# Kernel tuning notes

Measured on AMD Instinct MI355X. Metric: run time of the kernel, lower is better.

## Reference

```python
import jax, jax.numpy as jnp
import numpy as np

N = 50000      # nodes
E = 800000     # edges (avg degree 16)
IN_DIM = 256
OUT_DIM = 64
HEADS = 4
P_L = 0.1      # freq='low' slope


def setup_inputs() -> dict:
    key = jax.random.key(0)
    ks = jax.random.split(key, 12)
    h = jax.random.normal(ks[0], (N, IN_DIM), dtype=jnp.float32)
    src = jax.random.randint(ks[1], (E,), 0, N, dtype=jnp.int32)
    dst = jax.random.randint(ks[2], (E,), 0, N, dtype=jnp.int32)
    d = jax.random.uniform(ks[3], (N,), dtype=jnp.float32)  # degree norm per node
    s_in = 1.0 / np.sqrt(IN_DIM)
    s_d = 1.0 / np.sqrt(OUT_DIM)
    W_in = jax.random.normal(ks[4], (IN_DIM, HEADS * OUT_DIM), dtype=jnp.float32) * s_in
    b_in = jnp.zeros((HEADS * OUT_DIM,), dtype=jnp.float32)
    W_att = jax.random.normal(ks[5], (HEADS, OUT_DIM, OUT_DIM), dtype=jnp.float32) * s_d
    b_att = jnp.zeros((HEADS, OUT_DIM), dtype=jnp.float32)
    W_g = jax.random.normal(ks[6], (HEADS, 2 * OUT_DIM), dtype=jnp.float32) * s_d
    b_g = jnp.zeros((HEADS,), dtype=jnp.float32)
    W_out = jax.random.normal(ks[7], (HEADS * OUT_DIM, OUT_DIM), dtype=jnp.float32) * s_d
    b_out = jnp.zeros((OUT_DIM,), dtype=jnp.float32)
    return {"h": h, "src": src, "dst": dst, "d": d,
            "W_in": W_in, "b_in": b_in, "W_att": W_att, "b_att": b_att,
            "W_g": W_g, "b_g": b_g, "W_out": W_out, "b_out": b_out}


def reference(h, src, dst, d, W_in, b_in, W_att, b_att, W_g, b_g, W_out, b_out):
    # node transform: [N, H, D]  (dropout is identity in eval mode)
    hh = jax.nn.relu(h @ W_in + b_in).reshape(-1, HEADS, OUT_DIM)
    # per-head att_gate applied at node level (same math as per-edge, cheaper)
    a = jnp.einsum('nhd,hde->nhe', hh, W_att) + b_att           # [N, H, D]
    # gate linear on concat([dst_a, src_a]) split into the two halves of W_g
    g_dst = jnp.einsum('nhd,hd->nh', a, W_g[:, :OUT_DIM])        # [N, H]
    g_src = jnp.einsum('nhd,hd->nh', a, W_g[:, OUT_DIM:])        # [N, H]
    _h = g_dst[dst] + g_src[src] + b_g                           # [E, H]
    # freq='low': relu(where(_h>0, _h, -p_l*_h)) == where(_h>0, _h, -p_l*_h)
    g = jnp.where(_h > 0, _h, -P_L * _h)
    alpha = g * (d[dst] * d[src])[:, None]                       # [E, H]
    msg = hh[src] * alpha[..., None]                             # [E, H, D]
    z = jax.ops.segment_sum(msg, dst, num_segments=N)            # [N, H, D]
    return z.reshape(-1, HEADS * OUT_DIM) @ W_out + b_out        # [N, D]
```

## Files before the change

### kernel.cpp

```cpp
#include <hip/hip_runtime.h>
#include <hip/hip_bf16.h>

#define N_NODES 50000
#define N_EDGES 800000
#define IN_DIM 256
#define OUT_DIM 64
#define HEADS 4
#define HD 256
#define P_L 0.1f
#define TILE_N 64
#define CAP 64
#define OVCAP 4096

typedef __attribute__((ext_vector_type(8))) short bf16x8;
typedef __attribute__((ext_vector_type(4))) float f32x4;

static __device__ __forceinline__ short f2bf(float f) {
    __hip_bfloat16 b = __float2bfloat16(f);
    return *(short*)&b;
}

__global__ __launch_bounds__(256) void precompute_kernel(
    const float* __restrict__ W_att, const float* __restrict__ b_att,
    const float* __restrict__ W_g,
    float* __restrict__ v_dst, float* __restrict__ v_src,
    float* __restrict__ c_dst, float* __restrict__ c_src) {
    int t = threadIdx.x;
    int h = t >> 6, dd = t & 63;
    float sd = 0.f, ss = 0.f;
    for (int e = 0; e < 64; ++e) {
        float w = W_att[h * 4096 + dd * 64 + e];
        sd += w * W_g[h * 128 + e];
        ss += w * W_g[h * 128 + 64 + e];
    }
    v_dst[t] = sd;
    v_src[t] = ss;
    if (dd == 0) {
        float cd = 0.f, cs = 0.f;
        for (int e = 0; e < 64; ++e) {
            float b = b_att[h * 64 + e];
            cd += b * W_g[h * 128 + e];
            cs += b * W_g[h * 128 + 64 + e];
        }
        c_dst[h] = cd;
        c_src[h] = cs;
    }
}

__global__ __launch_bounds__(256) void wconv_kernel(
    const float* __restrict__ W_in, const float* __restrict__ W_out,
    short* __restrict__ W_bt, short* __restrict__ W_obt2) {
    int b = blockIdx.x, t = threadIdx.x;
    if (b < 256) {
        W_bt[t * 256 + b] = f2bf(W_in[b * 256 + t]);
    } else {
        int flat = (b - 256) * 256 + t;
        int k = flat & 63, oc = (flat >> 6) & 63, h = flat >> 12;
        W_obt2[flat] = f2bf(W_out[(h * 64 + k) * 64 + oc]);
    }
}

__global__ __launch_bounds__(256, 2) void node_mfma_kernel(
    const float* __restrict__ hin, const short* __restrict__ W_bt,
    const short* __restrict__ W_obt2, const float* __restrict__ b_in,
    const float* __restrict__ v_dst, const float* __restrict__ v_src,
    const float* __restrict__ c_dst, const float* __restrict__ c_src,
    __hip_bfloat16* __restrict__ y, float* __restrict__ gd,
    float* __restrict__ gs) {
    __shared__ short A_lds[TILE_N * 256];
    int t = threadIdx.x;
    int n0 = blockIdx.x * TILE_N;
    bool full = (n0 + TILE_N) <= N_NODES;

    #pragma unroll
    for (int rr = 0; rr < 4; ++rr) {
        int r = rr * 16 + (t >> 4), c0 = (t & 15) * 16;
        int row = n0 + r;
        if (row > N_NODES - 1) row = N_NODES - 1;
        const float* hp = hin + (size_t)row * IN_DIM + c0;
        float fv[16];
        *(float4*)&fv[0]  = *(const float4*)(hp + 0);
        *(float4*)&fv[4]  = *(const float4*)(hp + 4);
        *(float4*)&fv[8]  = *(const float4*)(hp + 8);
        *(float4*)&fv[12] = *(const float4*)(hp + 12);
        short sv[16];
        #pragma unroll
        for (int j = 0; j < 16; ++j) sv[j] = f2bf(fv[j]);
        int swz = (r & 7) << 3;
        int base = r * 256 + c0;
        *(bf16x8*)&A_lds[(base + 0) ^ swz] = *(bf16x8*)&sv[0];
        *(bf16x8*)&A_lds[(base + 8) ^ swz] = *(bf16x8*)&sv[8];
    }
    __syncthreads();

    int l = t & 63, w = t >> 6;
    int lr = l & 15, lg = l >> 4;
    int aswz = (lr & 7) << 3;

    f32x4 acc[4][4];
    #pragma unroll
    for (int rt = 0; rt < 4; ++rt)
        #pragma unroll
        for (int ct = 0; ct < 4; ++ct) acc[rt][ct] = (f32x4){0.f, 0.f, 0.f, 0.f};

    #pragma unroll
    for (int ks = 0; ks < 8; ++ks) {
        bf16x8 bfrag[4], afrag[4];
        #pragma unroll
        for (int ct = 0; ct < 4; ++ct)
            bfrag[ct] = *(const bf16x8*)(W_bt + (size_t)(w * 64 + ct * 16 + lr) * 256 + ks * 32 + lg * 8);
        #pragma unroll
        for (int rt = 0; rt < 4; ++rt)
            afrag[rt] = *(bf16x8*)&A_lds[((rt * 16 + lr) * 256 + ks * 32 + lg * 8) ^ aswz];
        #pragma unroll
        for (int rt = 0; rt < 4; ++rt)
            #pragma unroll
            for (int ct = 0; ct < 4; ++ct)
                acc[rt][ct] = __builtin_amdgcn_mfma_f32_16x16x32_bf16(afrag[rt], bfrag[ct], acc[rt][ct], 0, 0, 0);
    }

    int col[4];
    float vd[4], vs[4], bi[4];
    #pragma unroll
    for (int ct = 0; ct < 4; ++ct) {
        col[ct] = w * 64 + ct * 16 + lr;
        bi[ct] = b_in[col[ct]];
        vd[ct] = v_dst[col[ct]];
        vs[ct] = v_src[col[ct]];
    }
    float pd[4][4], ps[4][4];
    #pragma unroll
    for (int rt = 0; rt < 4; ++rt)
        #pragma unroll
        for (int r = 0; r < 4; ++r) { pd[rt][r] = 0.f; ps[rt][r] = 0.f; }
    #pragma unroll
    for (int rt = 0; rt < 4; ++rt)
        #pragma unroll
        for (int ct = 0; ct < 4; ++ct)
            #pragma unroll
            for (int r = 0; r < 4; ++r) {
                float v = fmaxf(acc[rt][ct][r] + bi[ct], 0.f);
                acc[rt][ct][r] = v;
                pd[rt][r] += v * vd[ct];
                ps[rt][r] += v * vs[ct];
            }
    #pragma unroll
    for (int rt = 0; rt < 4; ++rt)
        #pragma unroll
        for (int r = 0; r < 4; ++r) {
            #pragma unroll
            for (int off = 1; off < 16; off <<= 1) {
                pd[rt][r] += __shfl_xor(pd[rt][r], off, 64);
                ps[rt][r] += __shfl_xor(ps[rt][r], off, 64);
            }
        }
    if (lr == 0) {
        float cd = c_dst[w], cs = c_src[w];
        #pragma unroll
        for (int rt = 0; rt < 4; ++rt)
            #pragma unroll
            for (int r = 0; r < 4; ++r) {
                int m = rt * 16 + lg * 4 + r;
                if (full || (n0 + m) < N_NODES) {
                    gd[(n0 + m) * HEADS + w] = pd[rt][r] + cd;
                    gs[(n0 + m) * HEADS + w] = ps[rt][r] + cs;
                }
            }
    }

    __syncthreads();
    #pragma unroll
    for (int rt = 0; rt < 4; ++rt)
        #pragma unroll
        for (int ct = 0; ct < 4; ++ct)
            #pragma unroll
            for (int r = 0; r < 4; ++r) {
                int m = rt * 16 + lg * 4 + r;
                int idx = m * 256 + col[ct];
                A_lds[idx ^ (((lg * 4 + r) & 7) << 3)] = f2bf(acc[rt][ct][r]);
            }
    __syncthreads();

    f32x4 acc2[4][4];
    #pragma unroll
    for (int rt = 0; rt < 4; ++rt)
        #pragma unroll
        for (int ct = 0; ct < 4; ++ct) acc2[rt][ct] = (f32x4){0.f, 0.f, 0.f, 0.f};
    #pragma unroll
    for (int ks = 0; ks < 2; ++ks) {
        bf16x8 bfrag[4], afrag[4];
        #pragma unroll
        for (int ct = 0; ct < 4; ++ct)
            bfrag[ct] = *(const bf16x8*)(W_obt2 + (size_t)(w * 64 + ct * 16 + lr) * 64 + ks * 32 + lg * 8);
        #pragma unroll
        for (int rt = 0; rt < 4; ++rt)
            afrag[rt] = *(bf16x8*)&A_lds[((rt * 16 + lr) * 256 + w * 64 + ks * 32 + lg * 8) ^ aswz];
        #pragma unroll
        for (int rt = 0; rt < 4; ++rt)
            #pragma unroll
            for (int ct = 0; ct < 4; ++ct)
                acc2[rt][ct] = __builtin_amdgcn_mfma_f32_16x16x32_bf16(afrag[rt], bfrag[ct], acc2[rt][ct], 0, 0, 0);
    }
    #pragma unroll
    for (int rt = 0; rt < 4; ++rt)
        #pragma unroll
        for (int ct = 0; ct < 4; ++ct)
            #pragma unroll
            for (int r = 0; r < 4; ++r) {
                int m = rt * 16 + lg * 4 + r;
                if (full || (n0 + m) < N_NODES)
                    y[(size_t)(n0 + m) * HD + w * 64 + ct * 16 + lr] =
                        __float2bfloat16(acc2[rt][ct][r]);
            }
}

__global__ __launch_bounds__(256) void fill_kernel(
    const int* __restrict__ src, const int* __restrict__ dst,
    int* __restrict__ cursor, int* __restrict__ bucket_src,
    int* __restrict__ ov_list, int* __restrict__ ov_count) {
    int e = blockIdx.x * 256 + threadIdx.x;
    if (e >= N_EDGES) return;
    int n = dst[e];
    int pos = atomicAdd(&cursor[n], 1);
    if (pos < CAP) {
        bucket_src[(size_t)n * CAP + pos] = src[e];
    } else {
        int oi = atomicAdd(ov_count, 1);
        if (oi < OVCAP) ov_list[oi] = e;
    }
}

__global__ __launch_bounds__(256) void agg_kernel(
    const int* __restrict__ bucket_src, const int* __restrict__ cursor,
    const int* __restrict__ src, const int* __restrict__ dst,
    const int* __restrict__ ov_list, const int* __restrict__ ov_count,
    const float* __restrict__ dnorm, const float* __restrict__ b_g,
    const __hip_bfloat16* __restrict__ y, const float* __restrict__ gd,
    const float* __restrict__ gs, const float* __restrict__ b_out,
    float* __restrict__ out) {
    __shared__ float alpha_lds[4][CAP][HEADS];
    __shared__ int s_lds[4][CAP];
    int t = threadIdx.x;
    int wv = t >> 6, lane = t & 63;
    int n = blockIdx.x * 4 + wv;
    int deg = cursor[n];
    if (deg > CAP) deg = CAP;
    float dn = dnorm[n];

    int hd = lane & 3;
    float gdh = gd[n * HEADS + hd] + b_g[hd];
    #pragma unroll
    for (int it = 0; it < 4; ++it) {
        int ei = it * 16 + (lane >> 2);
        if (ei < deg) {
            int s = bucket_src[(size_t)n * CAP + ei];
            if (hd == 0) s_lds[wv][ei] = s;
            float _h = gdh + gs[s * HEADS + hd];
            float g = _h > 0.f ? _h : -P_L * _h;
            alpha_lds[wv][ei][hd] = g * dn * dnorm[s];
        }
    }
    __syncthreads();

    int h_l = lane >> 4;
    const unsigned int* yw = (const unsigned int*)y + lane * 2;
    float a0 = 0.f, a1 = 0.f, a2 = 0.f, a3 = 0.f;
    int i = 0;
    for (; i + 16 <= deg; i += 16) {
        uint2 v[16];
        float al[16];
        #pragma unroll
        for (int j = 0; j < 16; ++j) {
            int s = s_lds[wv][i + j];
            al[j] = alpha_lds[wv][i + j][h_l];
            v[j] = *(const uint2*)(yw + (size_t)s * 128);
        }
        #pragma unroll
        for (int j = 0; j < 16; ++j) {
            a0 += __uint_as_float(v[j].x << 16) * al[j];
            a1 += __uint_as_float(v[j].x & 0xffff0000u) * al[j];
            a2 += __uint_as_float(v[j].y << 16) * al[j];
            a3 += __uint_as_float(v[j].y & 0xffff0000u) * al[j];
        }
    }
    for (; i + 8 <= deg; i += 8) {
        uint2 v[8];
        float al[8];
        #pragma unroll
        for (int j = 0; j < 8; ++j) {
            int s = s_lds[wv][i + j];
            al[j] = alpha_lds[wv][i + j][h_l];
            v[j] = *(const uint2*)(yw + (size_t)s * 128);
        }
        #pragma unroll
        for (int j = 0; j < 8; ++j) {
            a0 += __uint_as_float(v[j].x << 16) * al[j];
            a1 += __uint_as_float(v[j].x & 0xffff0000u) * al[j];
            a2 += __uint_as_float(v[j].y << 16) * al[j];
            a3 += __uint_as_float(v[j].y & 0xffff0000u) * al[j];
        }
    }
    for (; i < deg; ++i) {
        int s = s_lds[wv][i];
        float al = alpha_lds[wv][i][h_l];
        uint2 vv = *(const uint2*)(yw + (size_t)s * 128);
        a0 += __uint_as_float(vv.x << 16) * al;
        a1 += __uint_as_float(vv.x & 0xffff0000u) * al;
        a2 += __uint_as_float(vv.y << 16) * al;
        a3 += __uint_as_float(vv.y & 0xffff0000u) * al;
    }

    int cnt = *ov_count;
    if (cnt > 0) {
        if (cnt > OVCAP) cnt = OVCAP;
        float gdh2 = gd[n * HEADS + h_l] + b_g[h_l];
        for (int j = 0; j < cnt; ++j) {
            int e = ov_list[j];
            if (dst[e] == n) {
                int s = src[e];
                float _h = gdh2 + gs[s * HEADS + h_l];
                float g = _h > 0.f ? _h : -P_L * _h;
                float al = g * dn * dnorm[s];
                uint2 vv = *(const uint2*)(yw + (size_t)s * 128);
                a0 += __uint_as_float(vv.x << 16) * al;
                a1 += __uint_as_float(vv.x & 0xffff0000u) * al;
                a2 += __uint_as_float(vv.y << 16) * al;
                a3 += __uint_as_float(vv.y & 0xffff0000u) * al;
            }
        }
    }

    a0 += __shfl_xor(a0, 16, 64); a0 += __shfl_xor(a0, 32, 64);
    a1 += __shfl_xor(a1, 16, 64); a1 += __shfl_xor(a1, 32, 64);
    a2 += __shfl_xor(a2, 16, 64); a2 += __shfl_xor(a2, 32, 64);
    a3 += __shfl_xor(a3, 16, 64); a3 += __shfl_xor(a3, 32, 64);
    if (lane < 16) {
        float4 bo = *(const float4*)&b_out[lane * 4];
        float4 o;
        o.x = a0 + bo.x; o.y = a1 + bo.y; o.z = a2 + bo.z; o.w = a3 + bo.w;
        *(float4*)&out[(size_t)n * OUT_DIM + lane * 4] = o;
    }
}

extern "C" void kernel_launch(void* const* d_in, const int* in_sizes, int n_in,
                              void* d_out, int out_size, void* d_ws, size_t ws_size,
                              hipStream_t stream) {
    const float* h     = (const float*)d_in[0];
    const int*   src   = (const int*)d_in[1];
    const int*   dst   = (const int*)d_in[2];
    const float* dnorm = (const float*)d_in[3];
    const float* W_in  = (const float*)d_in[4];
    const float* b_in  = (const float*)d_in[5];
    const float* W_att = (const float*)d_in[6];
    const float* b_att = (const float*)d_in[7];
    const float* W_g   = (const float*)d_in[8];
    const float* b_g   = (const float*)d_in[9];
    const float* W_out = (const float*)d_in[10];
    const float* b_out = (const float*)d_in[11];
    float* out = (float*)d_out;

    char* ws = (char*)d_ws;
    __hip_bfloat16* y = (__hip_bfloat16*)ws;
    ws += (size_t)N_NODES * HD * sizeof(__hip_bfloat16);
    float* gd    = (float*)ws;  ws += (size_t)N_NODES * HEADS * sizeof(float);
    float* gs    = (float*)ws;  ws += (size_t)N_NODES * HEADS * sizeof(float);
    float* v_dst = (float*)ws;  ws += 256 * sizeof(float);
    float* v_src = (float*)ws;  ws += 256 * sizeof(float);
    float* c_dst = (float*)ws;  ws += 16;
    float* c_src = (float*)ws;  ws += 16;
    int* cursor     = (int*)ws; ws += (size_t)N_NODES * sizeof(int);
    int* ov_count   = (int*)ws; ws += 16;
    int* ov_list    = (int*)ws; ws += OVCAP * sizeof(int);
    int* bucket_src = (int*)ws; ws += (size_t)N_NODES * CAP * sizeof(int);
    short* W_bt     = (short*)ws; ws += 256 * 256 * sizeof(short);
    short* W_obt2   = (short*)ws;

    hipMemsetAsync(cursor, 0, (size_t)N_NODES * sizeof(int), stream);
    hipMemsetAsync(ov_count, 0, sizeof(int), stream);

    precompute_kernel<<<1, 256, 0, stream>>>(W_att, b_att, W_g, v_dst, v_src, c_dst, c_src);
    wconv_kernel<<<320, 256, 0, stream>>>(W_in, W_out, W_bt, W_obt2);
    fill_kernel<<<(N_EDGES + 255) / 256, 256, 0, stream>>>(src, dst, cursor, bucket_src,
                                                           ov_list, ov_count);
    node_mfma_kernel<<<(N_NODES + TILE_N - 1) / TILE_N, 256, 0, stream>>>(
        h, W_bt, W_obt2, b_in, v_dst, v_src, c_dst, c_src, y, gd, gs);
    agg_kernel<<<N_NODES / 4, 256, 0, stream>>>(bucket_src, cursor, src, dst,
                                                ov_list, ov_count, dnorm, b_g,
                                                y, gd, gs, b_out, out);
}
```

Baseline: 183.2 us.

## Process two nodes per wavefront in aggregation with 16-byte gathers, no LDS staging

The aggregation kernel now maps two destination nodes onto each 64-lane wavefront, so each half-wave of 32 lanes covers one node. Each lane gathers a 16-byte chunk (8 bf16 values) of the 256-wide y row instead of 8 bytes. The LDS staging of per-edge alpha and source indices and the block barrier are removed; each lane recomputes alpha for its own head inline from gs and dnorm. This cuts the block-wide sync and the wasted lanes on low-degree nodes, at the cost of duplicated alpha math and loads across lanes and divergence when the two nodes in a wave have different degrees.

```diff
diff --git a/kernel.cpp b/kernel.cpp
--- a/kernel.cpp
+++ b/kernel.cpp
@@ -238,107 +238,91 @@
     const __hip_bfloat16* __restrict__ y, const float* __restrict__ gd,
     const float* __restrict__ gs, const float* __restrict__ b_out,
     float* __restrict__ out) {
-    __shared__ float alpha_lds[4][CAP][HEADS];
-    __shared__ int s_lds[4][CAP];
     int t = threadIdx.x;
     int wv = t >> 6, lane = t & 63;
-    int n = blockIdx.x * 4 + wv;
+    int half = lane >> 5, sl = lane & 31;
+    int n = blockIdx.x * 8 + wv * 2 + half;
+    int head = sl >> 3;
     int deg = cursor[n];
     if (deg > CAP) deg = CAP;
     float dn = dnorm[n];
-
-    int hd = lane & 3;
-    float gdh = gd[n * HEADS + hd] + b_g[hd];
-    #pragma unroll
-    for (int it = 0; it < 4; ++it) {
-        int ei = it * 16 + (lane >> 2);
-        if (ei < deg) {
-            int s = bucket_src[(size_t)n * CAP + ei];
-            if (hd == 0) s_lds[wv][ei] = s;
-            float _h = gdh + gs[s * HEADS + hd];
+    float gdh = gd[n * HEADS + head] + b_g[head];
+    int degmax = max(deg, __shfl_xor(deg, 32, 64));
+
+    const uint4* yb = (const uint4*)y;
+    const int* bp = bucket_src + (size_t)n * CAP;
+    float a[8];
+    #pragma unroll
+    for (int j = 0; j < 8; ++j) a[j] = 0.f;
+
+    for (int i = 0; i < degmax; i += 8) {
+        int sarr[8];
+        #pragma unroll
+        for (int j = 0; j < 8; ++j) {
+            int e = i + j;
+            sarr[j] = (e < deg) ? bp[e] : -1;
+        }
+        float gsv[8], dnv[8];
+        uint4 v[8];
+        #pragma unroll
+        for (int j = 0; j < 8; ++j) {
+            int s = sarr[j] < 0 ? 0 : sarr[j];
+            gsv[j] = gs[s * HEADS + head];
+            dnv[j] = dnorm[s];
+            v[j] = yb[(size_t)s * 32 + sl];
+        }
+        #pragma unroll
+        for (int j = 0; j < 8; ++j) {
+            float _h = gdh + gsv[j];
             float g = _h > 0.f ? _h : -P_L * _h;
-            alpha_lds[wv][ei][hd] = g * dn * dnorm[s];
-        }
-    }
-    __syncthreads();
-
-    int h_l = lane >> 4;
-    const unsigned int* yw = (const unsigned int*)y + lane * 2;
-    float a0 = 0.f, a1 = 0.f, a2 = 0.f, a3 = 0.f;
-    int i = 0;
-    for (; i + 16 <= deg; i += 16) {
-        uint2 v[16];
-        float al[16];
-        #pragma unroll
-        for (int j = 0; j < 16; ++j) {
-            int s = s_lds[wv][i + j];
-            al[j] = alpha_lds[wv][i + j][h_l];
-            v[j] = *(const uint2*)(yw + (size_t)s * 128);
-        }
-        #pragma unroll
-        for (int j = 0; j < 16; ++j) {
-            a0 += __uint_as_float(v[j].x << 16) * al[j];
-            a1 += __uint_as_float(v[j].x & 0xffff0000u) * al[j];
-            a2 += __uint_as_float(v[j].y << 16) * al[j];
-            a3 += __uint_as_float(v[j].y & 0xffff0000u) * al[j];
-        }
-    }
-    for (; i + 8 <= deg; i += 8) {
-        uint2 v[8];
-        float al[8];
-        #pragma unroll
-        for (int j = 0; j < 8; ++j) {
-            int s = s_lds[wv][i + j];
-            al[j] = alpha_lds[wv][i + j][h_l];
-            v[j] = *(const uint2*)(yw + (size_t)s * 128);
-        }
-        #pragma unroll
-        for (int j = 0; j < 8; ++j) {
-            a0 += __uint_as_float(v[j].x << 16) * al[j];
-            a1 += __uint_as_float(v[j].x & 0xffff0000u) * al[j];
-            a2 += __uint_as_float(v[j].y << 16) * al[j];
-            a3 += __uint_as_float(v[j].y & 0xffff0000u) * al[j];
-        }
-    }
-    for (; i < deg; ++i) {
-        int s = s_lds[wv][i];
-        float al = alpha_lds[wv][i][h_l];
-        uint2 vv = *(const uint2*)(yw + (size_t)s * 128);
-        a0 += __uint_as_float(vv.x << 16) * al;
-        a1 += __uint_as_float(vv.x & 0xffff0000u) * al;
-        a2 += __uint_as_float(vv.y << 16) * al;
-        a3 += __uint_as_float(vv.y & 0xffff0000u) * al;
+            float al = (sarr[j] < 0) ? 0.f : g * dn * dnv[j];
+            a[0] += __uint_as_float(v[j].x << 16) * al;
+            a[1] += __uint_as_float(v[j].x & 0xffff0000u) * al;
+            a[2] += __uint_as_float(v[j].y << 16) * al;
+            a[3] += __uint_as_float(v[j].y & 0xffff0000u) * al;
+            a[4] += __uint_as_float(v[j].z << 16) * al;
+            a[5] += __uint_as_float(v[j].z & 0xffff0000u) * al;
+            a[6] += __uint_as_float(v[j].w << 16) * al;
+            a[7] += __uint_as_float(v[j].w & 0xffff0000u) * al;
+        }
     }
 
     int cnt = *ov_count;
     if (cnt > 0) {
         if (cnt > OVCAP) cnt = OVCAP;
-        float gdh2 = gd[n * HEADS + h_l] + b_g[h_l];
         for (int j = 0; j < cnt; ++j) {
             int e = ov_list[j];
             if (dst[e] == n) {
                 int s = src[e];
-                float _h = gdh2 + gs[s * HEADS + h_l];
+                float _h = gdh + gs[s * HEADS + head];
                 float g = _h > 0.f ? _h : -P_L * _h;
                 float al = g * dn * dnorm[s];
-                uint2 vv = *(const uint2*)(yw + (size_t)s * 128);
-                a0 += __uint_as_float(vv.x << 16) * al;
-                a1 += __uint_as_float(vv.x & 0xffff0000u) * al;
-                a2 += __uint_as_float(vv.y << 16) * al;
-                a3 += __uint_as_float(vv.y & 0xffff0000u) * al;
-            }
-        }
-    }
-
-    a0 += __shfl_xor(a0, 16, 64); a0 += __shfl_xor(a0, 32, 64);
-    a1 += __shfl_xor(a1, 16, 64); a1 += __shfl_xor(a1, 32, 64);
-    a2 += __shfl_xor(a2, 16, 64); a2 += __shfl_xor(a2, 32, 64);
-    a3 += __shfl_xor(a3, 16, 64); a3 += __shfl_xor(a3, 32, 64);
-    if (lane < 16) {
-        float4 bo = *(const float4*)&b_out[lane * 4];
-        float4 o;
-        o.x = a0 + bo.x; o.y = a1 + bo.y; o.z = a2 + bo.z; o.w = a3 + bo.w;
-        *(float4*)&out[(size_t)n * OUT_DIM + lane * 4] = o;
+                uint4 vv = yb[(size_t)s * 32 + sl];
+                a[0] += __uint_as_float(vv.x << 16) * al;
+                a[1] += __uint_as_float(vv.x & 0xffff0000u) * al;
+                a[2] += __uint_as_float(vv.y << 16) * al;
+                a[3] += __uint_as_float(vv.y & 0xffff0000u) * al;
+                a[4] += __uint_as_float(vv.z << 16) * al;
+                a[5] += __uint_as_float(vv.z & 0xffff0000u) * al;
+                a[6] += __uint_as_float(vv.w << 16) * al;
+                a[7] += __uint_as_float(vv.w & 0xffff0000u) * al;
+            }
+        }
+    }
+
+    #pragma unroll
+    for (int j = 0; j < 8; ++j) {
+        a[j] += __shfl_xor(a[j], 8, 64);
+        a[j] += __shfl_xor(a[j], 16, 64);
+    }
+    if (sl < 8) {
+        float4 b0 = *(const float4*)&b_out[sl * 8];
+        float4 b1 = *(const float4*)&b_out[sl * 8 + 4];
+        float4 o0, o1;
+        o0.x = a[0] + b0.x; o0.y = a[1] + b0.y; o0.z = a[2] + b0.z; o0.w = a[3] + b0.w;
+        o1.x = a[4] + b1.x; o1.y = a[5] + b1.y; o1.z = a[6] + b1.z; o1.w = a[7] + b1.w;
+        *(float4*)&out[(size_t)n * OUT_DIM + sl * 8] = o0;
+        *(float4*)&out[(size_t)n * OUT_DIM + sl * 8 + 4] = o1;
     }
 }
 
@@ -384,7 +368,7 @@
                                                            ov_list, ov_count);
     node_mfma_kernel<<<(N_NODES + TILE_N - 1) / TILE_N, 256, 0, stream>>>(
         h, W_bt, W_obt2, b_in, v_dst, v_src, c_dst, c_src, y, gd, gs);
-    agg_kernel<<<N_NODES / 4, 256, 0, stream>>>(bucket_src, cursor, src, dst,
+    agg_kernel<<<N_NODES / 8, 256, 0, stream>>>(bucket_src, cursor, src, dst,
                                                 ov_list, ov_count, dnorm, b_g,
                                                 y, gd, gs, b_out, out);
 }
```

Result: faster. 169.4 us (-7.5%).
